# Optimization experiments

Measured on AMD Instinct MI355X. Metric: run time of the kernel, lower is better.

Reference implementation:

```python
import jax, jax.numpy as jnp
import numpy as np

D_MODEL = 1024
NUM_HEADS = 16
HEAD_DIM = D_MODEL // NUM_HEADS
THETA = 10000.0


def _init_linear(key, d_out, d_in):
    sigma = np.sqrt(2.0 / (d_in + d_out))
    w = jax.random.truncated_normal(key, -3.0, 3.0, (d_out, d_in), dtype=jnp.float32)
    return w * sigma


def setup_inputs() -> dict:
    key = jax.random.key(0)
    kh, kq, kk, kv, ko = jax.random.split(key, 5)
    h = jax.random.normal(kh, (2, 2048, D_MODEL), dtype=jnp.float32)
    return {
        "h": h,
        "wq": _init_linear(kq, D_MODEL, D_MODEL),
        "wk": _init_linear(kk, D_MODEL, D_MODEL),
        "wv": _init_linear(kv, D_MODEL, D_MODEL),
        "wo": _init_linear(ko, D_MODEL, D_MODEL),
    }


def _rope(x, pos):
    # x: [B, H, T, dh]; rotate interleaved pairs (..., 2k, 2k+1)
    dh = x.shape[-1]
    freq = THETA ** (-jnp.arange(0, dh // 2, dtype=jnp.float32) / (dh // 2))
    ang = pos[:, None] * freq[None, :]            # [T, dh/2]
    cos, sin = jnp.cos(ang), jnp.sin(ang)
    xr = x.reshape(*x.shape[:-1], dh // 2, 2)
    x0, x1 = xr[..., 0], xr[..., 1]
    out = jnp.stack((cos * x0 - sin * x1, sin * x0 + cos * x1), axis=-1)
    return out.reshape(x.shape)


def reference(h, wq, wk, wv, wo):
    B, T, D = h.shape
    Hn, dh = NUM_HEADS, HEAD_DIM

    def split_heads(x):  # [B,T,D] -> [B,H,T,dh]
        return x.reshape(B, T, Hn, dh).transpose(0, 2, 1, 3)

    Q = split_heads(h @ wq.T)
    K = split_heads(h @ wk.T)
    V = split_heads(h @ wv.T)

    pos = jnp.arange(T, dtype=jnp.float32)
    Q = _rope(Q, pos)
    K = _rope(K, pos)

    scores = jnp.einsum('bhqd,bhkd->bhqk', Q, K) / jnp.sqrt(jnp.float32(dh))
    mask = jnp.tril(jnp.ones((T, T), dtype=bool))
    scores = jnp.where(mask, scores, -jnp.inf)
    attn = jax.nn.softmax(scores, axis=-1)
    out = jnp.einsum('bhqk,bhkd->bhqd', attn, V)   # [B,H,T,dh]
    out = out.transpose(0, 2, 1, 3).reshape(B, T, D)
    return out @ wo.T
```

## Files before the change

### kernel.cpp

```cpp
#include <hip/hip_runtime.h>
#include <math.h>

typedef __bf16 bf16_t;
typedef __bf16 v8bf __attribute__((ext_vector_type(8)));
typedef __bf16 v4bf __attribute__((ext_vector_type(4)));
typedef float  v4f  __attribute__((ext_vector_type(4)));

#define AS1 __attribute__((address_space(1)))
#define AS3 __attribute__((address_space(3)))

static __device__ __forceinline__ void load_lds16(const bf16_t* g, bf16_t* l) {
    __builtin_amdgcn_global_load_lds((AS1 void*)const_cast<bf16_t*>(g),
                                     (AS3 void*)l, 16, 0, 0);
}
static __device__ __forceinline__ void load_lds16b(const char* g, char* l) {
    __builtin_amdgcn_global_load_lds((AS1 void*)const_cast<char*>(g),
                                     (AS3 void*)l, 16, 0, 0);
}

static __device__ __forceinline__ void fast_sincos(float ang, float* sn, float* cs) {
    float rv = ang * 0.15915494309189535f;
    rv -= floorf(rv);
    const float a = rv * 6.283185307179586f;
    *sn = __sinf(a);
    *cs = __cosf(a);
}

__global__ __launch_bounds__(256) void cvt_fp32_bf16(
    const float* __restrict__ h,  const float* __restrict__ wq,
    const float* __restrict__ wk, const float* __restrict__ wv,
    const float* __restrict__ wo,
    bf16_t* __restrict__ hb,  bf16_t* __restrict__ wqb,
    bf16_t* __restrict__ wkb, bf16_t* __restrict__ wvb,
    bf16_t* __restrict__ wob)
{
    const size_t HM = (size_t)4 << 20;
    const size_t i8 = ((size_t)blockIdx.x * 256 + threadIdx.x) * 8;
    const float* src; bf16_t* dst; size_t off;
    if (i8 < HM) { src = h; dst = hb; off = i8; }
    else {
        const size_t r = (i8 - HM) >> 20;
        off = (i8 - HM) & (((size_t)1 << 20) - 1);
        src = (r == 0) ? wq  : (r == 1) ? wk  : (r == 2) ? wv  : wo;
        dst = (r == 0) ? wqb : (r == 1) ? wkb : (r == 2) ? wvb : wob;
    }
    const float4 a = *(const float4*)(src + off);
    const float4 b = *(const float4*)(src + off + 4);
    v8bf o;
    o[0]=(bf16_t)a.x; o[1]=(bf16_t)a.y; o[2]=(bf16_t)a.z; o[3]=(bf16_t)a.w;
    o[4]=(bf16_t)b.x; o[5]=(bf16_t)b.y; o[6]=(bf16_t)b.z; o[7]=(bf16_t)b.w;
    *(v8bf*)(dst + off) = o;
}

__global__ __launch_bounds__(256) void qkv_gemm_rope(
    const bf16_t* __restrict__ A,
    const bf16_t* __restrict__ wq,
    const bf16_t* __restrict__ wk,
    const bf16_t* __restrict__ wv,
    bf16_t* __restrict__ qo, bf16_t* __restrict__ ko, bf16_t* __restrict__ vo)
{
    __shared__ __align__(16) bf16_t smem[17408];

    const int tid = threadIdx.x;
    const int n0  = blockIdx.x * 128;
    const int m0  = blockIdx.y * 128;
    const int sel = n0 >> 10;
    const bf16_t* W = (sel == 0) ? wq : (sel == 1) ? wk : wv;
    const int wr0 = n0 & 1023;

    const int wave = tid >> 6;
    const int lane = tid & 63;
    const int l16  = lane & 15;
    const int quad = lane >> 4;
    const int wrow = (wave >> 1) * 64;
    const int wcol = (wave & 1) * 64;

    v4f acc[4][4];
    #pragma unroll
    for (int i = 0; i < 4; ++i)
        #pragma unroll
        for (int j = 0; j < 4; ++j) acc[i][j] = (v4f)(0.0f);

    const int c0r  = tid >> 2;
    const int c0c  = (tid & 3) * 8;
    #define QKV_STAGE(bbuf, ktile)                                             \
        {                                                                      \
            const int k0_ = (ktile) * 32;                                      \
            load_lds16(A + (size_t)(m0 + c0r) * 1024 + k0_ + c0c,              \
                       smem + (bbuf) * 4096 + tid * 8);                        \
            load_lds16(A + (size_t)(m0 + 64 + c0r) * 1024 + k0_ + c0c,         \
                       smem + (bbuf) * 4096 + 2048 + tid * 8);                 \
            load_lds16(W + (size_t)(wr0 + c0r) * 1024 + k0_ + c0c,             \
                       smem + 8192 + (bbuf) * 4096 + tid * 8);                 \
            load_lds16(W + (size_t)(wr0 + 64 + c0r) * 1024 + k0_ + c0c,        \
                       smem + 8192 + (bbuf) * 4096 + 2048 + tid * 8);          \
        }

    QKV_STAGE(0, 0);
    for (int kt = 0; kt < 32; ++kt) {
        const int cur = kt & 1;
        __syncthreads();
        if (kt < 31) QKV_STAGE(cur ^ 1, kt + 1);

        const bf16_t* As = smem + cur * 4096;
        const bf16_t* Bs = smem + 8192 + cur * 4096;
        v8bf af[4], bfb[4];
        #pragma unroll
        for (int i = 0; i < 4; ++i) {
            af[i]  = *(const v8bf*)&As[(wrow + i * 16 + l16) * 32 + quad * 8];
            bfb[i] = *(const v8bf*)&Bs[(wcol + i * 16 + l16) * 32 + quad * 8];
        }
        #pragma unroll
        for (int i = 0; i < 4; ++i)
            #pragma unroll
            for (int j = 0; j < 4; ++j)
                acc[i][j] = __builtin_amdgcn_mfma_f32_16x16x32_bf16(
                    af[i], bfb[j], acc[i][j], 0, 0, 0);
    }
    __syncthreads();
    #undef QKV_STAGE

    bf16_t* Ls = smem + wave * 4352;
    const int bq     = (m0 + wrow) >> 11;
    const int hd     = ((n0 + wcol) >> 6) & 15;
    const int t_base = (m0 + wrow) & 2047;

    if (sel < 2) {
        bf16_t* OUT = (sel == 0) ? qo : ko;
        #pragma unroll
        for (int j = 0; j < 4; ++j) {
            const int dcol = j * 16 + l16;
            const int kk   = dcol >> 1;
            const float f  = exp2f((float)kk * -0.4152410118609203f);
            float cb, sb, c1, s1, c16, s16;
            fast_sincos((float)(t_base + quad * 4) * f, &sb, &cb);
            fast_sincos(f, &s1, &c1);
            fast_sincos(16.0f * f, &s16, &c16);
            float ci = cb, si = sb;
            #pragma unroll
            for (int i = 0; i < 4; ++i) {
                float cr = ci, sr = si;
                #pragma unroll
                for (int r = 0; r < 4; ++r) {
                    const int mrow = i * 16 + quad * 4 + r;
                    float v = acc[i][j][r];
                    const float vp = __shfl_xor(v, 1);
                    v = ((dcol & 1) == 0) ? (cr * v - sr * vp)
                                          : (sr * vp + cr * v);
                    Ls[mrow * 68 + dcol] = (bf16_t)v;
                    if (r < 3) {
                        const float cn = cr * c1 - sr * s1;
                        sr = sr * c1 + cr * s1;
                        cr = cn;
                    }
                }
                if (i < 3) {
                    const float cn = ci * c16 - si * s16;
                    si = si * c16 + ci * s16;
                    ci = cn;
                }
            }
        }
        #pragma unroll
        for (int s = 0; s < 8; ++s) {
            const int row = s * 8 + (lane >> 3);
            const int off = (lane & 7) * 8;
            const v8bf vv = *(const v8bf*)&Ls[row * 68 + off];
            *(v8bf*)(OUT + (((size_t)(bq * 16 + hd) * 2048) + t_base + row) * 64 + off) = vv;
        }
    } else {
        #pragma unroll
        for (int i = 0; i < 4; ++i)
            #pragma unroll
            for (int j = 0; j < 4; ++j) {
                v4bf p;
                #pragma unroll
                for (int r = 0; r < 4; ++r) p[r] = (bf16_t)acc[i][j][r];
                *(v4bf*)&Ls[(j * 16 + l16) * 68 + i * 16 + quad * 4] = p;
            }
        #pragma unroll
        for (int s = 0; s < 8; ++s) {
            const int drow = s * 8 + (lane >> 3);
            const int off  = (lane & 7) * 8;
            const v8bf vv = *(const v8bf*)&Ls[drow * 68 + off];
            *(v8bf*)(vo + (((size_t)(bq * 16 + hd) * 64) + drow) * 2048 + t_base + off) = vv;
        }
    }
}

__global__ __launch_bounds__(256, 4) void attn_mfma(
    const bf16_t* __restrict__ qg,
    const bf16_t* __restrict__ kg,
    const bf16_t* __restrict__ vtg,
    bf16_t* __restrict__ og)
{
    __shared__ __align__(16) bf16_t Ks[2][4096];
    __shared__ __align__(16) bf16_t Vs[2][4096];
    __shared__ __align__(16) bf16_t Ps[4][1024];

    const int tid  = threadIdx.x;
    const int wave = tid >> 6;
    const int lane = tid & 63;
    const int l16  = lane & 15;
    const int quad = lane >> 4;

    const int i   = blockIdx.x;
    const int xcd = i & 7;
    const int j   = i >> 3;
    const int bhl = j >> 5;
    const int u   = j & 31;
    const int q64 = (bhl & 1) ? (31 - u) : u;
    const int bh  = xcd * 4 + bhl;
    const int b = bh >> 4, hh = bh & 15;

    const char* Kb = (const char*)(kg  + (size_t)bh * 2048 * 64);
    const char* Vb = (const char*)(vtg + (size_t)bh * 64 * 2048);

    const int qglb = q64 * 64 + wave * 16 + l16;

    const int sw  = (l16 & 7) << 4;
    const int cb0 = (quad << 4) ^ sw;

    const int grow = tid >> 3;
    const int gsw  = ((tid & 7) << 4) ^ ((grow & 7) << 4);

    const bf16_t* qrow = qg + ((size_t)bh * 2048 + qglb) * 64;
    v8bf qf[2];
    qf[0] = *(const v8bf*)(qrow + quad * 8);
    qf[1] = *(const v8bf*)(qrow + 32 + quad * 8);
    #pragma unroll
    for (int e = 0; e < 8; ++e) {
        qf[0][e] = (bf16_t)((float)qf[0][e] * 0.18033688011112042f);
        qf[1][e] = (bf16_t)((float)qf[1][e] * 0.18033688011112042f);
    }

    v8bf ones1;
    #pragma unroll
    for (int e = 0; e < 8; ++e) ones1[e] = (bf16_t)1.0f;

    float m_r = -1e30f;
    v4f l_acc = (v4f)(0.0f);
    v4f o_acc[4];
    #pragma unroll
    for (int d = 0; d < 4; ++d) o_acc[d] = (v4f)(0.0f);

    {
        const char* ks = Kb + ((size_t)grow << 7) + gsw;
        const char* vs = Vb + ((size_t)grow << 12) + gsw;
        char* kd = (char*)Ks[0] + tid * 16;
        char* vd = (char*)Vs[0] + tid * 16;
        load_lds16b(ks, kd);
        load_lds16b(ks + (32 << 7), kd + 4096);
        load_lds16b(vs, vd);
        load_lds16b(vs + ((size_t)32 << 12), vd + 4096);
    }

    for (int kt = 0; kt <= q64; ++kt) {
        const int cur = kt & 1;
        const int nxt = cur ^ 1;
        __syncthreads();

        if (kt < q64) {
            const char* ks = Kb + ((size_t)((kt + 1) * 64 + grow) << 7) + gsw;
            const char* vs = Vb + ((size_t)grow << 12) + ((size_t)(kt + 1) << 7) + gsw;
            char* kd = (char*)Ks[nxt] + tid * 16;
            char* vd = (char*)Vs[nxt] + tid * 16;
            load_lds16b(ks, kd);
            load_lds16b(ks + (32 << 7), kd + 4096);
            load_lds16b(vs, vd);
            load_lds16b(vs + ((size_t)32 << 12), vd + 4096);
        }

        const char* ksc = (const char*)Ks[cur];
        v4f s_acc[4];
        #pragma unroll
        for (int kblk = 0; kblk < 4; ++kblk) s_acc[kblk] = (v4f)(0.0f);
        v8bf kfr[4][2];
        #pragma unroll
        for (int kblk = 0; kblk < 4; ++kblk) {
            const char* kr = ksc + ((kblk * 16 + l16) << 7);
            kfr[kblk][0] = *(const v8bf*)(kr + cb0);
            kfr[kblk][1] = *(const v8bf*)(kr + (cb0 ^ 64));
        }
        __builtin_amdgcn_s_setprio(1);
        #pragma unroll
        for (int kblk = 0; kblk < 4; ++kblk) {
            s_acc[kblk] = __builtin_amdgcn_mfma_f32_16x16x32_bf16(
                kfr[kblk][0], qf[0], s_acc[kblk], 0, 0, 0);
            s_acc[kblk] = __builtin_amdgcn_mfma_f32_16x16x32_bf16(
                kfr[kblk][1], qf[1], s_acc[kblk], 0, 0, 0);
        }
        __builtin_amdgcn_s_setprio(0);

        const char* vsc = (const char*)Vs[cur];
        v8bf vfr[4][2];
        #pragma unroll
        for (int dblk = 0; dblk < 4; ++dblk) {
            const char* vr = vsc + ((dblk * 16 + l16) << 7);
            vfr[dblk][0] = *(const v8bf*)(vr + cb0);
            vfr[dblk][1] = *(const v8bf*)(vr + (cb0 ^ 64));
        }

        if (kt == q64) {
            #pragma unroll
            for (int kblk = 0; kblk < 4; ++kblk)
                #pragma unroll
                for (int r = 0; r < 4; ++r)
                    if (kt * 64 + kblk * 16 + quad * 4 + r > qglb)
                        s_acc[kblk][r] = -1e30f;
        }

        float m01 = fmaxf(fmaxf(s_acc[0][0], s_acc[0][1]),
                          fmaxf(s_acc[0][2], s_acc[0][3]));
        float m23 = fmaxf(fmaxf(s_acc[1][0], s_acc[1][1]),
                          fmaxf(s_acc[1][2], s_acc[1][3]));
        float m45 = fmaxf(fmaxf(s_acc[2][0], s_acc[2][1]),
                          fmaxf(s_acc[2][2], s_acc[2][3]));
        float m67 = fmaxf(fmaxf(s_acc[3][0], s_acc[3][1]),
                          fmaxf(s_acc[3][2], s_acc[3][3]));
        float mx = fmaxf(fmaxf(m01, m23), fmaxf(m45, m67));
        mx = fmaxf(mx, __shfl_xor(mx, 16));
        mx = fmaxf(mx, __shfl_xor(mx, 32));
        if (!__all(mx - m_r <= 8.0f)) {
            const float mn = fmaxf(m_r, mx);
            const float a  = exp2f(m_r - mn);
            m_r = mn;
            l_acc *= a;
            #pragma unroll
            for (int d = 0; d < 4; ++d) o_acc[d] *= a;
        }

        char* psc = (char*)Ps[wave] + (l16 << 7);
        #pragma unroll
        for (int kblk = 0; kblk < 4; ++kblk) {
            v4bf p;
            #pragma unroll
            for (int r = 0; r < 4; ++r)
                p[r] = (bf16_t)exp2f(s_acc[kblk][r] - m_r);
            *(v4bf*)(psc + ((kblk * 32 + quad * 8) ^ sw)) = p;
        }
        const v8bf pf0 = *(const v8bf*)(psc + cb0);
        const v8bf pf1 = *(const v8bf*)(psc + (cb0 ^ 64));

        __builtin_amdgcn_s_setprio(1);
        #pragma unroll
        for (int dblk = 0; dblk < 4; ++dblk) {
            o_acc[dblk] = __builtin_amdgcn_mfma_f32_16x16x32_bf16(
                vfr[dblk][0], pf0, o_acc[dblk], 0, 0, 0);
            o_acc[dblk] = __builtin_amdgcn_mfma_f32_16x16x32_bf16(
                vfr[dblk][1], pf1, o_acc[dblk], 0, 0, 0);
        }
        l_acc = __builtin_amdgcn_mfma_f32_16x16x32_bf16(ones1, pf0, l_acc, 0, 0, 0);
        l_acc = __builtin_amdgcn_mfma_f32_16x16x32_bf16(ones1, pf1, l_acc, 0, 0, 0);
        __builtin_amdgcn_s_setprio(0);
    }

    const float inv_l = 1.0f / l_acc[0];
    const size_t base = ((size_t)b * 2048 + qglb) * 1024 + hh * 64;
    #pragma unroll
    for (int dblk = 0; dblk < 4; ++dblk) {
        v4bf o;
        #pragma unroll
        for (int r = 0; r < 4; ++r) o[r] = (bf16_t)(o_acc[dblk][r] * inv_l);
        *(v4bf*)(og + base + dblk * 16 + quad * 4) = o;
    }
}

__global__ __launch_bounds__(256) void out_gemm(
    const bf16_t* __restrict__ A,
    const bf16_t* __restrict__ W,
    float* __restrict__ C)
{
    __shared__ __align__(16) float smemf[6144];
    bf16_t* Sb = (bf16_t*)smemf;

    const int tid = threadIdx.x;
    const int n0  = blockIdx.x * 64;
    const int m0  = blockIdx.y * 128;

    const int wave = tid >> 6;
    const int lane = tid & 63;
    const int l16  = lane & 15;
    const int quad = lane >> 4;
    const int wrow = (wave >> 1) * 64;
    const int wcol = (wave & 1) * 32;

    v4f acc[4][2];
    #pragma unroll
    for (int i = 0; i < 4; ++i)
        #pragma unroll
        for (int j = 0; j < 2; ++j) acc[i][j] = (v4f)(0.0f);

    const int c0r = tid >> 2;
    const int c0c = (tid & 3) * 8;
    #define OUT_STAGE(bbuf, ktile)                                             \
        {                                                                      \
            const int k0_ = (ktile) * 32;                                      \
            load_lds16(A + (size_t)(m0 + c0r) * 1024 + k0_ + c0c,              \
                       Sb + (bbuf) * 4096 + tid * 8);                          \
            load_lds16(A + (size_t)(m0 + 64 + c0r) * 1024 + k0_ + c0c,         \
                       Sb + (bbuf) * 4096 + 2048 + tid * 8);                   \
            load_lds16(W + (size_t)(n0 + (tid >> 2)) * 1024 + k0_ + c0c,       \
                       Sb + 8192 + (bbuf) * 2048 + tid * 8);                   \
        }

    OUT_STAGE(0, 0);
    for (int kt = 0; kt < 32; ++kt) {
        const int cur = kt & 1;
        __syncthreads();
        if (kt < 31) OUT_STAGE(cur ^ 1, kt + 1);

        const bf16_t* As = Sb + cur * 4096;
        const bf16_t* Bs = Sb + 8192 + cur * 2048;
        v8bf af[4], bfb[2];
        #pragma unroll
        for (int i = 0; i < 4; ++i)
            af[i]  = *(const v8bf*)&As[(wrow + i * 16 + l16) * 32 + quad * 8];
        #pragma unroll
        for (int j = 0; j < 2; ++j)
            bfb[j] = *(const v8bf*)&Bs[(wcol + j * 16 + l16) * 32 + quad * 8];
        #pragma unroll
        for (int i = 0; i < 4; ++i)
            #pragma unroll
            for (int j = 0; j < 2; ++j)
                acc[i][j] = __builtin_amdgcn_mfma_f32_16x16x32_bf16(
                    af[i], bfb[j], acc[i][j], 0, 0, 0);
    }
    __syncthreads();
    #undef OUT_STAGE

    float* Lw = smemf + wave * 1088;
    #pragma unroll
    for (int half = 0; half < 2; ++half) {
        #pragma unroll
        for (int ii = 0; ii < 2; ++ii) {
            const int i = half * 2 + ii;
            #pragma unroll
            for (int j = 0; j < 2; ++j)
                #pragma unroll
                for (int r = 0; r < 4; ++r)
                    Lw[(ii * 16 + quad * 4 + r) * 34 + j * 16 + l16] = acc[i][j][r];
        }
        #pragma unroll
        for (int s = 0; s < 8; ++s) {
            const int row = s * 4 + (lane >> 4);
            const float2 vv = *(const float2*)&Lw[row * 34 + l16 * 2];
            *(float2*)(C + (size_t)(m0 + wrow + half * 32 + row) * 1024
                         + n0 + wcol + l16 * 2) = vv;
        }
    }
}

extern "C" void kernel_launch(void* const* d_in, const int* in_sizes, int n_in,
                              void* d_out, int out_size, void* d_ws, size_t ws_size,
                              hipStream_t stream) {
    const float* h  = (const float*)d_in[0];
    const float* wq = (const float*)d_in[1];
    const float* wk = (const float*)d_in[2];
    const float* wv = (const float*)d_in[3];
    const float* wo = (const float*)d_in[4];

    const size_t NH = (size_t)4096 * 1024;
    const size_t NW = (size_t)1024 * 1024;

    bf16_t* hb  = (bf16_t*)d_ws;
    bf16_t* wqb = hb  + NH;
    bf16_t* wkb = wqb + NW;
    bf16_t* wvb = wkb + NW;
    bf16_t* wob = wvb + NW;
    bf16_t* qw  = wob + NW;
    bf16_t* kw  = qw + NH;
    bf16_t* vw  = kw + NH;
    bf16_t* og  = hb;

    cvt_fp32_bf16<<<dim3(4096), dim3(256), 0, stream>>>(
        h, wq, wk, wv, wo, hb, wqb, wkb, wvb, wob);
    qkv_gemm_rope<<<dim3(24, 32), dim3(256), 0, stream>>>(
        hb, wqb, wkb, wvb, qw, kw, vw);
    attn_mfma<<<dim3(1024), dim3(256), 0, stream>>>(qw, kw, vw, og);
    out_gemm<<<dim3(16, 32), dim3(256), 0, stream>>>(og, wob, (float*)d_out);
}
```

Baseline: 187.1 us.

## Transpose softmax probabilities in registers via permlane swaps instead of LDS

Replaces the per-wave LDS round-trip that re-laid out the bf16 probability tile from the accumulator layout into the MFMA B-operand layout. It now packs pairs with v_cvt_pk_bf16_f32 and shuffles them across lanes with v_permlane32_swap and ds_swizzle. It also interleaves the K-fragment LDS reads with the QK MFMAs and drops the s_setprio hints. This removes LDS writes, reads and the 8KB Ps buffer, which may help occupancy, but the cross-lane permutation has to reproduce the previous swizzled layout exactly or results will be wrong.

```diff
diff --git a/kernel.cpp b/kernel.cpp
--- a/kernel.cpp
+++ b/kernel.cpp
@@ -196,7 +196,6 @@
 {
     __shared__ __align__(16) bf16_t Ks[2][4096];
     __shared__ __align__(16) bf16_t Vs[2][4096];
-    __shared__ __align__(16) bf16_t Ps[4][1024];
 
     const int tid  = threadIdx.x;
     const int wave = tid >> 6;
@@ -275,22 +274,16 @@
         v4f s_acc[4];
         #pragma unroll
         for (int kblk = 0; kblk < 4; ++kblk) s_acc[kblk] = (v4f)(0.0f);
-        v8bf kfr[4][2];
         #pragma unroll
         for (int kblk = 0; kblk < 4; ++kblk) {
             const char* kr = ksc + ((kblk * 16 + l16) << 7);
-            kfr[kblk][0] = *(const v8bf*)(kr + cb0);
-            kfr[kblk][1] = *(const v8bf*)(kr + (cb0 ^ 64));
-        }
-        __builtin_amdgcn_s_setprio(1);
-        #pragma unroll
-        for (int kblk = 0; kblk < 4; ++kblk) {
+            const v8bf kf0 = *(const v8bf*)(kr + cb0);
+            const v8bf kf1 = *(const v8bf*)(kr + (cb0 ^ 64));
             s_acc[kblk] = __builtin_amdgcn_mfma_f32_16x16x32_bf16(
-                kfr[kblk][0], qf[0], s_acc[kblk], 0, 0, 0);
+                kf0, qf[0], s_acc[kblk], 0, 0, 0);
             s_acc[kblk] = __builtin_amdgcn_mfma_f32_16x16x32_bf16(
-                kfr[kblk][1], qf[1], s_acc[kblk], 0, 0, 0);
-        }
-        __builtin_amdgcn_s_setprio(0);
+                kf1, qf[1], s_acc[kblk], 0, 0, 0);
+        }
 
         const char* vsc = (const char*)Vs[cur];
         v8bf vfr[4][2];
@@ -330,29 +323,44 @@
             for (int d = 0; d < 4; ++d) o_acc[d] *= a;
         }
 
-        char* psc = (char*)Ps[wave] + (l16 << 7);
+        unsigned w[4][2];
         #pragma unroll
         for (int kblk = 0; kblk < 4; ++kblk) {
-            v4bf p;
-            #pragma unroll
-            for (int r = 0; r < 4; ++r)
-                p[r] = (bf16_t)exp2f(s_acc[kblk][r] - m_r);
-            *(v4bf*)(psc + ((kblk * 32 + quad * 8) ^ sw)) = p;
-        }
-        const v8bf pf0 = *(const v8bf*)(psc + cb0);
-        const v8bf pf1 = *(const v8bf*)(psc + (cb0 ^ 64));
-
-        __builtin_amdgcn_s_setprio(1);
+            #pragma unroll
+            for (int h2 = 0; h2 < 2; ++h2) {
+                const float e0 = exp2f(s_acc[kblk][2 * h2]     - m_r);
+                const float e1 = exp2f(s_acc[kblk][2 * h2 + 1] - m_r);
+                asm("v_cvt_pk_bf16_f32 %0, %1, %2"
+                    : "=v"(w[kblk][h2]) : "v"(e0), "v"(e1));
+            }
+        }
+
+        union PF { unsigned u[4]; v8bf v; } pf[2];
+        #pragma unroll
+        for (int g = 0; g < 2; ++g) {
+            #pragma unroll
+            for (int h2 = 0; h2 < 2; ++h2) {
+                unsigned a = w[g * 2][h2];
+                unsigned bb = w[g * 2 + 1][h2];
+                asm("v_permlane32_swap_b32 %0, %1" : "+v"(a), "+v"(bb));
+                const unsigned aswz = __builtin_amdgcn_ds_swizzle(a, 0x401F);
+                const unsigned bswz = __builtin_amdgcn_ds_swizzle(bb, 0x401F);
+                pf[g].u[h2]     = (lane & 16) ? bswz : a;
+                pf[g].u[2 + h2] = (lane & 16) ? bb   : aswz;
+            }
+        }
+
         #pragma unroll
         for (int dblk = 0; dblk < 4; ++dblk) {
             o_acc[dblk] = __builtin_amdgcn_mfma_f32_16x16x32_bf16(
-                vfr[dblk][0], pf0, o_acc[dblk], 0, 0, 0);
+                vfr[dblk][0], pf[0].v, o_acc[dblk], 0, 0, 0);
             o_acc[dblk] = __builtin_amdgcn_mfma_f32_16x16x32_bf16(
-                vfr[dblk][1], pf1, o_acc[dblk], 0, 0, 0);
-        }
-        l_acc = __builtin_amdgcn_mfma_f32_16x16x32_bf16(ones1, pf0, l_acc, 0, 0, 0);
-        l_acc = __builtin_amdgcn_mfma_f32_16x16x32_bf16(ones1, pf1, l_acc, 0, 0, 0);
-        __builtin_amdgcn_s_setprio(0);
+                vfr[dblk][1], pf[1].v, o_acc[dblk], 0, 0, 0);
+        }
+        l_acc = __builtin_amdgcn_mfma_f32_16x16x32_bf16(
+            ones1, pf[0].v, l_acc, 0, 0, 0);
+        l_acc = __builtin_amdgcn_mfma_f32_16x16x32_bf16(
+            ones1, pf[1].v, l_acc, 0, 0, 0);
     }
 
     const float inv_l = 1.0f / l_acc[0];
```

New measurement: 185.9 us. No clear change (-0.6%).
